# Optimization experiments

Measured on AMD Instinct MI355X. Metric: run time of the kernel, lower is better.

Reference implementation:

```python
import jax, jax.numpy as jnp
import numpy as np

B, L, D_MODEL = 4, 4096, 128
D_INNER, D_STATE, DT_RANK, D_CONV = 256, 16, 8, 4
EPS = 1e-5


def setup_inputs() -> dict:
    key = jax.random.key(0)
    ks = jax.random.split(key, 10)
    s = lambda *sh: 0.02
    inp = {
        'x': jax.random.normal(ks[0], (B, L, D_MODEL), jnp.float32),
        'norm_w': jnp.ones((D_MODEL,), jnp.float32),
        # Linear weights stored as (in, out) so y = x @ W
        'in_proj_w': jax.random.normal(ks[1], (D_MODEL, 2 * D_INNER), jnp.float32) * 0.02,
        'conv_w': jax.random.normal(ks[2], (D_INNER, D_CONV), jnp.float32) * 0.2,
        'conv_b': jnp.zeros((D_INNER,), jnp.float32),
        'x_proj_w': jax.random.normal(ks[3], (D_INNER, DT_RANK + 2 * D_STATE), jnp.float32) * 0.02,
        'dt_proj_w': jax.random.normal(ks[4], (DT_RANK, D_INNER), jnp.float32) * 0.1,
        'dt_proj_b': jnp.zeros((D_INNER,), jnp.float32),
        'A_log': jnp.log(jnp.tile(jnp.arange(1, D_STATE + 1, dtype=jnp.float32)[None, :], (D_INNER, 1))),
        'D': jnp.ones((D_INNER,), jnp.float32),
        'out_proj_w': jax.random.normal(ks[5], (D_INNER, D_MODEL), jnp.float32) * 0.02,
    }
    return inp


def _mamba_block(x, norm_w, in_proj_w, conv_w, conv_b, x_proj_w,
                 dt_proj_w, dt_proj_b, A_log, D, out_proj_w):
    b, l, d = x.shape
    # RMSNorm
    h = x * jax.lax.rsqrt(jnp.mean(x * x, axis=-1, keepdims=True) + EPS) * norm_w
    # in_proj -> split into x path and residual gate
    xr = h @ in_proj_w                      # (b, l, 2*d_inner)
    xi, res = jnp.split(xr, 2, axis=-1)
    # depthwise causal conv1d over time
    xc = jnp.transpose(xi, (0, 2, 1))       # (b, d_inner, l)
    kernel = conv_w[:, None, :]             # (d_inner, 1, d_conv)
    xc = jax.lax.conv_general_dilated(
        xc, kernel, window_strides=(1,), padding=[(D_CONV - 1, 0)],
        feature_group_count=D_INNER,
        dimension_numbers=('NCH', 'OIH', 'NCH')) + conv_b[None, :, None]
    xc = jnp.transpose(xc, (0, 2, 1))       # (b, l, d_inner)
    xc = jax.nn.silu(xc)
    # SSM parameterization
    A = -jnp.exp(A_log.astype(jnp.float32))           # (d_inner, n)
    x_dbl = xc @ x_proj_w                              # (b, l, dt_rank + 2n)
    delta = x_dbl[..., :DT_RANK]
    Bmat = x_dbl[..., DT_RANK:DT_RANK + D_STATE]       # (b, l, n)
    Cmat = x_dbl[..., DT_RANK + D_STATE:]              # (b, l, n)
    delta = jax.nn.softplus(delta @ dt_proj_w + dt_proj_b)  # (b, l, d_inner)
    # discretize
    deltaA = jnp.exp(jnp.einsum('bld,dn->bldn', delta, A))  # (b, l, d_inner, n)
    deltaB_u = delta[..., None] * Bmat[:, :, None, :] * xc[..., None]
    # selective scan over time (lax.scan replaces the Python loop)
    def step(s, inputs):
        dA_t, dBu_t, C_t = inputs
        s = dA_t * s + dBu_t                     # (b, d_inner, n)
        y_t = jnp.einsum('bdn,bn->bd', s, C_t)   # (b, d_inner)
        return s, y_t
    s0 = jnp.zeros((b, D_INNER, D_STATE), xc.dtype)
    scan_in = (jnp.transpose(deltaA, (1, 0, 2, 3)),
               jnp.transpose(deltaB_u, (1, 0, 2, 3)),
               jnp.transpose(Cmat, (1, 0, 2)))
    _, ys = jax.lax.scan(step, s0, scan_in)      # (l, b, d_inner)
    y = jnp.transpose(ys, (1, 0, 2)) + xc * D    # (b, l, d_inner)
    y = y * jax.nn.silu(res)
    return y @ out_proj_w + x                    # residual add


def reference(x, norm_w, in_proj_w, conv_w, conv_b, x_proj_w,
              dt_proj_w, dt_proj_b, A_log, D, out_proj_w):
    return _mamba_block(x, norm_w, in_proj_w, conv_w, conv_b, x_proj_w,
                        dt_proj_w, dt_proj_b, A_log, D, out_proj_w)
```

## Files before the change

kernel.cpp:

```cpp
#include <hip/hip_runtime.h>
#include <math.h>

#define B_    4
#define L_    4096
#define DM    128
#define DI    256
#define DS    16
#define DTR   8
#define XPN   (DTR + 2*DS)
#define NB    (DI + 2*DS)
#define M_    (B_*L_)
#define CHUNK 32
#define NC    (L_/CHUNK)
#define LOG2E 1.4426950408889634f
#define PREP_N (512*128 + NB*DI + DM*DI)

typedef __attribute__((ext_vector_type(8))) short bf16x8;
typedef __attribute__((ext_vector_type(4))) float f32x4;
typedef unsigned short ushort_t;

__device__ __forceinline__ ushort_t f2bf(float f) {
  unsigned int u = __float_as_uint(f);
  u += 0x7FFFu + ((u >> 16) & 1u);
  return (ushort_t)(u >> 16);
}
__device__ __forceinline__ float bf2f(ushort_t u) {
  return __uint_as_float(((unsigned int)u) << 16);
}

__global__ __launch_bounds__(256) void prep_rms_kernel(const float* __restrict__ x,
                                                       const float* __restrict__ nw,
                                                       const float* __restrict__ inW,
                                                       const float* __restrict__ Wx,
                                                       const float* __restrict__ Wdt,
                                                       const float* __restrict__ outw,
                                                       ushort_t* __restrict__ xbf,
                                                       ushort_t* __restrict__ inWt,
                                                       ushort_t* __restrict__ WbigT,
                                                       ushort_t* __restrict__ outWt) {
  if (blockIdx.x < M_ / 4) {
    int row  = blockIdx.x * 4 + (threadIdx.x >> 6);
    int lane = threadIdx.x & 63;
    const float* xp = x + (size_t)row * DM;
    float v0 = xp[lane], v1 = xp[lane + 64];
    float s = v0 * v0 + v1 * v1;
    #pragma unroll
    for (int off = 32; off > 0; off >>= 1) s += __shfl_xor(s, off);
    float r = rsqrtf(s / DM + 1e-5f);
    ushort_t* op = xbf + (size_t)row * DM;
    op[lane]      = f2bf(v0 * r * nw[lane]);
    op[lane + 64] = f2bf(v1 * r * nw[lane + 64]);
    return;
  }
  int g = (blockIdx.x - M_ / 4) * 256 + threadIdx.x;
  if (g < 512 * 128) {
    int n = g >> 7, k = g & 127;
    inWt[g] = f2bf(inW[k * 512 + n]);
  } else if (g < 512 * 128 + NB * DI) {
    int q = g - 512 * 128;
    int c = q >> 8, k = q & 255;
    float v;
    if (c < DI) {
      v = 0.f;
      #pragma unroll
      for (int j = 0; j < DTR; ++j) v = fmaf(Wx[k * XPN + j], Wdt[j * DI + c], v);
    } else {
      v = Wx[k * XPN + DTR + (c - DI)];
    }
    WbigT[q] = f2bf(v);
  } else if (g < PREP_N) {
    int q = g - (512 * 128 + NB * DI);
    int n = q >> 8, k = q & 255;
    outWt[q] = f2bf(outw[k * DM + n]);
  }
}

__global__ __launch_bounds__(256) void g1_conv_kernel(const ushort_t* __restrict__ A,
                                                      const ushort_t* __restrict__ Wt,
                                                      const float* __restrict__ cw,
                                                      const float* __restrict__ cb,
                                                      ushort_t* __restrict__ xcbf,
                                                      ushort_t* __restrict__ resbf) {
  constexpr int BM = 128, BN = 64, BK = 64, KK = 128, NT = BN / 16;
  __shared__ __align__(16) char smem_raw[35648];
  ushort_t (*Asm)[145][8] = (ushort_t (*)[145][8])smem_raw;
  ushort_t (*Bsm)[65][8]  = (ushort_t (*)[65][8])(smem_raw + 18560);
  float* T = (float*)smem_raw;
  const int tid  = threadIdx.x;
  const int wave = tid >> 6, lane = tid & 63;
  const int quad = lane >> 4, l16 = lane & 15;
  const int row0 = blockIdx.x * BM;
  const int by   = blockIdx.y;
  const int col0 = by * BN;
  const bool zpad = (row0 & (L_ - 1)) == 0;
  f32x4 acc[2][NT], acc2[NT];
  #pragma unroll
  for (int mt = 0; mt < 2; ++mt)
    #pragma unroll
    for (int nt = 0; nt < NT; ++nt) acc[mt][nt] = (f32x4){0.f, 0.f, 0.f, 0.f};
  #pragma unroll
  for (int nt = 0; nt < NT; ++nt) acc2[nt] = (f32x4){0.f, 0.f, 0.f, 0.f};

  for (int k0 = 0; k0 < KK; k0 += BK) {
    #pragma unroll
    for (int i = 0; i < 5; ++i) {
      int q = tid + i * 256;
      if (i < 4 || tid < 128) {
        int m = q >> 3, kb = q & 7;
        bf16x8 v = {0, 0, 0, 0, 0, 0, 0, 0};
        if (!(zpad && m < 16))
          v = *(const bf16x8*)(A + (size_t)(row0 - 16 + m) * KK + k0 + kb * 8);
        *(bf16x8*)(&Asm[kb][m][0]) = v;
      }
    }
    #pragma unroll
    for (int i = 0; i < 2; ++i) {
      int q = tid + i * 256;
      int n = q >> 3, kb = q & 7;
      *(bf16x8*)(&Bsm[kb][n][0]) =
          *(const bf16x8*)(Wt + (size_t)(col0 + n) * KK + k0 + kb * 8);
    }
    __syncthreads();
    #pragma unroll
    for (int ks = 0; ks < 2; ++ks) {
      bf16x8 af[2], bfr[NT];
      #pragma unroll
      for (int mt = 0; mt < 2; ++mt)
        af[mt] = *(const bf16x8*)(&Asm[ks * 4 + quad][16 + wave * 32 + mt * 16 + l16][0]);
      #pragma unroll
      for (int nt = 0; nt < NT; ++nt)
        bfr[nt] = *(const bf16x8*)(&Bsm[ks * 4 + quad][nt * 16 + l16][0]);
      #pragma unroll
      for (int mt = 0; mt < 2; ++mt)
        #pragma unroll
        for (int nt = 0; nt < NT; ++nt)
          acc[mt][nt] = __builtin_amdgcn_mfma_f32_16x16x32_bf16(af[mt], bfr[nt],
                                                                acc[mt][nt], 0, 0, 0);
      if (by < 4 && wave == 0) {
        bf16x8 ab = *(const bf16x8*)(&Asm[ks * 4 + quad][l16][0]);
        #pragma unroll
        for (int nt = 0; nt < NT; ++nt)
          acc2[nt] = __builtin_amdgcn_mfma_f32_16x16x32_bf16(ab, bfr[nt],
                                                             acc2[nt], 0, 0, 0);
      }
    }
    __syncthreads();
  }

  if (by < 4) {
    #pragma unroll
    for (int mt = 0; mt < 2; ++mt)
      #pragma unroll
      for (int nt = 0; nt < NT; ++nt)
        #pragma unroll
        for (int r = 0; r < 4; ++r)
          T[(3 + wave * 32 + mt * 16 + quad * 4 + r) * 68 + nt * 16 + l16] =
              acc[mt][nt][r];
    if (wave == 0 && quad == 3) {
      #pragma unroll
      for (int nt = 0; nt < NT; ++nt)
        #pragma unroll
        for (int r = 1; r < 4; ++r)
          T[(r - 1) * 68 + nt * 16 + l16] = acc2[nt][r];
    }
    __syncthreads();
    const int c   = tid & 63;
    const int R0  = (tid >> 6) * 32;
    const int dch = col0 + c;
    float4 w4   = *(const float4*)(cw + dch * 4);
    float bias  = cb[dch];
    float t0 = T[(R0 + 0) * 68 + c];
    float t1 = T[(R0 + 1) * 68 + c];
    float t2 = T[(R0 + 2) * 68 + c];
    for (int rr = 0; rr < 32; ++rr) {
      float t3 = T[(R0 + rr + 3) * 68 + c];
      float s = fmaf(w4.x, t0, fmaf(w4.y, t1, fmaf(w4.z, t2, fmaf(w4.w, t3, bias))));
      float v = s / (1.f + __expf(-s));
      xcbf[(size_t)(row0 + R0 + rr) * DI + dch] = f2bf(v);
      t0 = t1; t1 = t2; t2 = t3;
    }
  } else {
    const int cr = col0 - 256;
    #pragma unroll
    for (int mt = 0; mt < 2; ++mt)
      #pragma unroll
      for (int nt = 0; nt < NT; ++nt) {
        int col   = cr + nt * 16 + l16;
        int rbase = row0 + wave * 32 + mt * 16 + quad * 4;
        #pragma unroll
        for (int r = 0; r < 4; ++r)
          resbf[(size_t)(rbase + r) * DI + col] = f2bf(acc[mt][nt][r]);
      }
  }
}

__global__ __launch_bounds__(512, 4) void scanA_kernel(
    const ushort_t* __restrict__ xcbf, const ushort_t* __restrict__ WbigT,
    const float* __restrict__ bdt, const float* __restrict__ Alog,
    ushort_t* __restrict__ deltab, ushort_t* __restrict__ Bmb,
    ushort_t* __restrict__ Cmb, float2* __restrict__ PS) {
  __shared__ __align__(16) ushort_t Asm[32][33][8];
  __shared__ float T[32][257];
  __shared__ float Bs[32][17], Cs[32][17];
  const int tid  = threadIdx.x;
  const int wave = tid >> 6, lane = tid & 63;
  const int quad = lane >> 4, l16 = lane & 15;
  const int b = blockIdx.x >> 7, c = blockIdx.x & (NC - 1);
  const size_t rowbase = (size_t)b * L_ + (size_t)c * CHUNK;
  const int d  = (wave << 5) | (lane & 31);
  const int nh = lane >> 5;
  const int n0 = nh * 8;

  {
    int m = tid & 31, kb = tid >> 5;
    *(bf16x8*)(&Asm[kb][m][0]) =
        *(const bf16x8*)(xcbf + (rowbase + m) * DI + kb * 8);
    *(bf16x8*)(&Asm[kb + 16][m][0]) =
        *(const bf16x8*)(xcbf + (rowbase + m) * DI + (kb + 16) * 8);
  }
  __syncthreads();

  for (int tp = wave; tp < 36; tp += 8) {
    int mt = tp / 18, nt = tp % 18;
    f32x4 acc = {0.f, 0.f, 0.f, 0.f};
    #pragma unroll
    for (int ks = 0; ks < 8; ++ks) {
      bf16x8 af = *(const bf16x8*)(&Asm[ks * 4 + quad][mt * 16 + l16][0]);
      bf16x8 bf = *(const bf16x8*)(WbigT + (size_t)(nt * 16 + l16) * DI + ks * 32 + quad * 8);
      acc = __builtin_amdgcn_mfma_f32_16x16x32_bf16(af, bf, acc, 0, 0, 0);
    }
    int row = mt * 16 + quad * 4;
    if (nt < 16) {
      int col = nt * 16 + l16;
      float bb = bdt[col];
      #pragma unroll
      for (int r = 0; r < 4; ++r) {
        float v = acc[r] + bb;
        T[row + r][col] = (v > 20.f) ? v : log1pf(__expf(v));
      }
    } else if (nt == 16) {
      #pragma unroll
      for (int r = 0; r < 4; ++r) Bs[row + r][l16] = acc[r];
    } else {
      #pragma unroll
      for (int r = 0; r < 4; ++r) Cs[row + r][l16] = acc[r];
    }
  }
  __syncthreads();

  #pragma unroll
  for (int i = 0; i < 8; ++i) {
    int idx2 = tid + i * 512;
    int row = idx2 >> 7, cp = idx2 & 127;
    unsigned int pk = (unsigned int)f2bf(T[row][2 * cp]) |
                      ((unsigned int)f2bf(T[row][2 * cp + 1]) << 16);
    *(unsigned int*)(deltab + (rowbase + row) * DI + 2 * cp) = pk;
  }
  {
    int row = tid >> 4, n = tid & 15;
    Bmb[rowbase * DS + tid] = f2bf(Bs[row][n]);
    Cmb[rowbase * DS + tid] = f2bf(Cs[row][n]);
  }

  float c0 = -__expf(Alog[d * DS]) * LOG2E;
  float aln[8];
  #pragma unroll
  for (int j = 0; j < 8; ++j) aln[j] = -__expf(Alog[d * DS + n0 + j]) * LOG2E;
  bool geom = true;
  #pragma unroll
  for (int j = 0; j < 8; ++j)
    geom = geom && (fabsf(aln[j] - (n0 + j + 1) * c0) <= 1e-3f * fabsf(aln[j]));

  float P[8], S[8];
  #pragma unroll
  for (int j = 0; j < 8; ++j) { P[j] = 1.f; S[j] = 0.f; }
  for (int t = 0; t < CHUNK; ++t) {
    float dl = T[t][d];
    float xv = bf2f(Asm[d >> 3][t][d & 7]);
    float du = dl * xv;
    if (geom) {
      float e1 = exp2f(dl * c0);
      float a;
      if (nh) { float e2 = e1 * e1, e4 = e2 * e2; a = e4 * e4 * e1; }
      else a = e1;
      #pragma unroll
      for (int j = 0; j < 8; ++j) {
        P[j] *= a;
        S[j] = fmaf(a, S[j], du * Bs[t][n0 + j]);
        a *= e1;
      }
    } else {
      #pragma unroll
      for (int j = 0; j < 8; ++j) {
        float a = exp2f(dl * aln[j]);
        P[j] *= a;
        S[j] = fmaf(a, S[j], du * Bs[t][n0 + j]);
      }
    }
  }
  size_t ob = ((size_t)(b * NC + c) << 12) + ((nh * 256 + d) << 3);
  float4* p4 = (float4*)(PS + ob);
  p4[0] = make_float4(P[0], S[0], P[1], S[1]);
  p4[1] = make_float4(P[2], S[2], P[3], S[3]);
  p4[2] = make_float4(P[4], S[4], P[5], S[5]);
  p4[3] = make_float4(P[6], S[6], P[7], S[7]);
}

__global__ __launch_bounds__(64) void scanB_kernel(const float2* __restrict__ PS,
                                                   float* __restrict__ sinit) {
  int g  = blockIdx.x * 64 + threadIdx.x;
  int b  = g >> 12;
  int dn = g & 4095;
  float s = 0.f;
  #pragma unroll 8
  for (int c = 0; c < NC; ++c) {
    size_t idx = ((size_t)(b * NC + c) << 12) + dn;
    sinit[idx] = s;
    float2 v = PS[idx];
    s = fmaf(v.x, s, v.y);
  }
}

__global__ __launch_bounds__(512, 4) void scanC_kernel(
    const ushort_t* __restrict__ deltab, const ushort_t* __restrict__ xcbf,
    const ushort_t* __restrict__ Bmb, const ushort_t* __restrict__ Cmb,
    const float* __restrict__ Alog, const float* __restrict__ Dp,
    const ushort_t* __restrict__ resbf, const float* __restrict__ sinit,
    const ushort_t* __restrict__ outWt, const float* __restrict__ x,
    float* __restrict__ out) {
  __shared__ float Bs[32][17], Cs[32][17];
  __shared__ __align__(16) ushort_t y2s[32][264];
  const int tid  = threadIdx.x;
  const int wave = tid >> 6, lane = tid & 63;
  const int quad = lane >> 4, l16 = lane & 15;
  const int b = blockIdx.x >> 7, c = blockIdx.x & (NC - 1);
  const size_t rowbase = (size_t)b * L_ + (size_t)c * CHUNK;
  const int d  = (wave << 5) | (lane & 31);
  const int nh = lane >> 5;
  const int n0 = nh * 8;
  {
    int row = tid >> 4, n = tid & 15;
    Bs[row][n] = bf2f(Bmb[rowbase * DS + tid]);
    Cs[row][n] = bf2f(Cmb[rowbase * DS + tid]);
  }
  float c0 = -__expf(Alog[d * DS]) * LOG2E;
  float aln[8];
  #pragma unroll
  for (int j = 0; j < 8; ++j) aln[j] = -__expf(Alog[d * DS + n0 + j]) * LOG2E;
  bool geom = true;
  #pragma unroll
  for (int j = 0; j < 8; ++j)
    geom = geom && (fabsf(aln[j] - (n0 + j + 1) * c0) <= 1e-3f * fabsf(aln[j]));
  const float Dd = Dp[d];
  float S[8];
  {
    size_t ib = ((size_t)(b * NC + c) << 12) + ((nh * 256 + d) << 3);
    float4 v0 = *(const float4*)(sinit + ib);
    float4 v1 = *(const float4*)(sinit + ib + 4);
    S[0] = v0.x; S[1] = v0.y; S[2] = v0.z; S[3] = v0.w;
    S[4] = v1.x; S[5] = v1.y; S[6] = v1.z; S[7] = v1.w;
  }
  __syncthreads();
  for (int t = 0; t < CHUNK; ++t) {
    float dl = bf2f(deltab[(rowbase + t) * DI + d]);
    float xv = bf2f(xcbf[(rowbase + t) * DI + d]);
    float du = dl * xv;
    float y = 0.f;
    if (geom) {
      float e1 = exp2f(dl * c0);
      float a;
      if (nh) { float e2 = e1 * e1, e4 = e2 * e2; a = e4 * e4 * e1; }
      else a = e1;
      #pragma unroll
      for (int j = 0; j < 8; ++j) {
        S[j] = fmaf(a, S[j], du * Bs[t][n0 + j]);
        y = fmaf(S[j], Cs[t][n0 + j], y);
        a *= e1;
      }
    } else {
      #pragma unroll
      for (int j = 0; j < 8; ++j) {
        float a = exp2f(dl * aln[j]);
        S[j] = fmaf(a, S[j], du * Bs[t][n0 + j]);
        y = fmaf(S[j], Cs[t][n0 + j], y);
      }
    }
    float yo = __shfl_xor(y, 32);
    if (nh == 0) {
      float rv = bf2f(resbf[(rowbase + t) * DI + d]);
      float yt = y + yo + xv * Dd;
      float sil = rv / (1.f + __expf(-rv));
      y2s[t][d] = f2bf(yt * sil);
    }
  }
  __syncthreads();
  #pragma unroll
  for (int mt = 0; mt < 2; ++mt) {
    f32x4 acc = {0.f, 0.f, 0.f, 0.f};
    #pragma unroll
    for (int ks = 0; ks < 8; ++ks) {
      bf16x8 af = *(const bf16x8*)(&y2s[mt * 16 + l16][ks * 32 + quad * 8]);
      bf16x8 bf = *(const bf16x8*)(outWt + (size_t)(wave * 16 + l16) * DI + ks * 32 + quad * 8);
      acc = __builtin_amdgcn_mfma_f32_16x16x32_bf16(af, bf, acc, 0, 0, 0);
    }
    int col = wave * 16 + l16;
    size_t rb = rowbase + mt * 16 + quad * 4;
    #pragma unroll
    for (int r = 0; r < 4; ++r)
      out[(rb + r) * DM + col] = acc[r] + x[(rb + r) * DM + col];
  }
}

extern "C" void kernel_launch(void* const* d_in, const int* in_sizes, int n_in,
                              void* d_out, int out_size, void* d_ws, size_t ws_size,
                              hipStream_t stream) {
  const float* x      = (const float*)d_in[0];
  const float* norm_w = (const float*)d_in[1];
  const float* inW    = (const float*)d_in[2];
  const float* convw  = (const float*)d_in[3];
  const float* convb  = (const float*)d_in[4];
  const float* xprojw = (const float*)d_in[5];
  const float* dtw    = (const float*)d_in[6];
  const float* dtb    = (const float*)d_in[7];
  const float* alog   = (const float*)d_in[8];
  const float* Dp     = (const float*)d_in[9];
  const float* outw   = (const float*)d_in[10];
  float* out = (float*)d_out;

  const size_t CS = (size_t)B_ * NC * DI * DS;
  float2* PS    = (float2*)d_ws;
  float* sinit  = (float*)(PS + CS);
  ushort_t* bfbase = (ushort_t*)(sinit + CS);
  ushort_t* xbf    = bfbase;
  ushort_t* xcbf   = xbf + (size_t)M_ * DM;
  ushort_t* resbf  = xcbf + (size_t)M_ * DI;
  ushort_t* deltab = resbf + (size_t)M_ * DI;
  ushort_t* Bmb    = deltab + (size_t)M_ * DI;
  ushort_t* Cmb    = Bmb + (size_t)M_ * DS;
  ushort_t* inWt   = Cmb + (size_t)M_ * DS;
  ushort_t* WbigT  = inWt + 512 * 128;
  ushort_t* outWt  = WbigT + NB * DI;

  prep_rms_kernel<<<M_ / 4 + (PREP_N + 255) / 256, 256, 0, stream>>>(
      x, norm_w, inW, xprojw, dtw, outw, xbf, inWt, WbigT, outWt);
  g1_conv_kernel<<<dim3(M_ / 128, 8), 256, 0, stream>>>(
      xbf, inWt, convw, convb, xcbf, resbf);
  scanA_kernel<<<B_ * NC, 512, 0, stream>>>(
      xcbf, WbigT, dtb, alog, deltab, Bmb, Cmb, PS);
  scanB_kernel<<<(B_ * DI * DS) / 64, 64, 0, stream>>>(PS, sinit);
  scanC_kernel<<<B_ * NC, 512, 0, stream>>>(
      deltab, xcbf, Bmb, Cmb, alog, Dp, resbf, sinit, outWt, x, out);
}
```

Measured before the change: 169.4 us.

## Fuse RMSNorm into in_proj GEMM and pack scan chunk summaries as bf16

RMSNorm moves out of the prep kernel and into the in_proj/conv GEMM. Each block now reads fp32 x directly, computes per-row scales, and writes normalized bf16 rows into shared memory across the full K=128, which removes the intermediate xbf buffer round trip. The cost is that each block redoes the norm for its rows and halo, 8 column blocks per row tile, and needs more LDS. The per-chunk (P,S) summaries passed from scanA to scanB are also packed into bf16 pairs to halve that traffic, which adds precision loss to the carried state, and the scanB unroll rises from 8 to 16.

```diff
diff --git a/kernel.cpp b/kernel.cpp
--- a/kernel.cpp
+++ b/kernel.cpp
@@ -13,11 +13,12 @@
 #define CHUNK 32
 #define NC    (L_/CHUNK)
 #define LOG2E 1.4426950408889634f
-#define PREP_N (512*128 + NB*DI + DM*DI)
+#define PREPW_N (512*128 + NB*DI + DM*DI)
 
 typedef __attribute__((ext_vector_type(8))) short bf16x8;
 typedef __attribute__((ext_vector_type(4))) float f32x4;
 typedef unsigned short ushort_t;
+typedef unsigned int uint_t;
 
 __device__ __forceinline__ ushort_t f2bf(float f) {
   unsigned int u = __float_as_uint(f);
@@ -27,32 +28,18 @@
 __device__ __forceinline__ float bf2f(ushort_t u) {
   return __uint_as_float(((unsigned int)u) << 16);
 }
-
-__global__ __launch_bounds__(256) void prep_rms_kernel(const float* __restrict__ x,
-                                                       const float* __restrict__ nw,
-                                                       const float* __restrict__ inW,
-                                                       const float* __restrict__ Wx,
-                                                       const float* __restrict__ Wdt,
-                                                       const float* __restrict__ outw,
-                                                       ushort_t* __restrict__ xbf,
-                                                       ushort_t* __restrict__ inWt,
-                                                       ushort_t* __restrict__ WbigT,
-                                                       ushort_t* __restrict__ outWt) {
-  if (blockIdx.x < M_ / 4) {
-    int row  = blockIdx.x * 4 + (threadIdx.x >> 6);
-    int lane = threadIdx.x & 63;
-    const float* xp = x + (size_t)row * DM;
-    float v0 = xp[lane], v1 = xp[lane + 64];
-    float s = v0 * v0 + v1 * v1;
-    #pragma unroll
-    for (int off = 32; off > 0; off >>= 1) s += __shfl_xor(s, off);
-    float r = rsqrtf(s / DM + 1e-5f);
-    ushort_t* op = xbf + (size_t)row * DM;
-    op[lane]      = f2bf(v0 * r * nw[lane]);
-    op[lane + 64] = f2bf(v1 * r * nw[lane + 64]);
-    return;
-  }
-  int g = (blockIdx.x - M_ / 4) * 256 + threadIdx.x;
+__device__ __forceinline__ uint_t pack2(float p, float s) {
+  return (uint_t)f2bf(p) | ((uint_t)f2bf(s) << 16);
+}
+
+__global__ __launch_bounds__(256) void prep_w_kernel(const float* __restrict__ inW,
+                                                     const float* __restrict__ Wx,
+                                                     const float* __restrict__ Wdt,
+                                                     const float* __restrict__ outw,
+                                                     ushort_t* __restrict__ inWt,
+                                                     ushort_t* __restrict__ WbigT,
+                                                     ushort_t* __restrict__ outWt) {
+  int g = blockIdx.x * 256 + threadIdx.x;
   if (g < 512 * 128) {
     int n = g >> 7, k = g & 127;
     inWt[g] = f2bf(inW[k * 512 + n]);
@@ -68,31 +55,68 @@
       v = Wx[k * XPN + DTR + (c - DI)];
     }
     WbigT[q] = f2bf(v);
-  } else if (g < PREP_N) {
+  } else if (g < PREPW_N) {
     int q = g - (512 * 128 + NB * DI);
     int n = q >> 8, k = q & 255;
     outWt[q] = f2bf(outw[k * DM + n]);
   }
 }
 
-__global__ __launch_bounds__(256) void g1_conv_kernel(const ushort_t* __restrict__ A,
+__global__ __launch_bounds__(256) void g1_conv_kernel(const float* __restrict__ x,
+                                                      const float* __restrict__ nw,
                                                       const ushort_t* __restrict__ Wt,
                                                       const float* __restrict__ cw,
                                                       const float* __restrict__ cb,
                                                       ushort_t* __restrict__ xcbf,
                                                       ushort_t* __restrict__ resbf) {
-  constexpr int BM = 128, BN = 64, BK = 64, KK = 128, NT = BN / 16;
-  __shared__ __align__(16) char smem_raw[35648];
+  constexpr int NT = 4;
+  __shared__ __align__(16) char smem_raw[46528];
   ushort_t (*Asm)[145][8] = (ushort_t (*)[145][8])smem_raw;
-  ushort_t (*Bsm)[65][8]  = (ushort_t (*)[65][8])(smem_raw + 18560);
-  float* T = (float*)smem_raw;
+  ushort_t (*Bsm)[65][8]  = (ushort_t (*)[65][8])(smem_raw + 37120);
+  float* scl = (float*)(smem_raw + 45440);
+  float* nwS = (float*)(smem_raw + 46016);
+  float* T   = (float*)smem_raw;
   const int tid  = threadIdx.x;
   const int wave = tid >> 6, lane = tid & 63;
   const int quad = lane >> 4, l16 = lane & 15;
-  const int row0 = blockIdx.x * BM;
+  const int row0 = blockIdx.x * 128;
   const int by   = blockIdx.y;
-  const int col0 = by * BN;
+  const int col0 = by * 64;
   const bool zpad = (row0 & (L_ - 1)) == 0;
+
+  if (tid < 32) ((float4*)nwS)[tid] = ((const float4*)nw)[tid];
+  for (int i = 0; i < 18; ++i) {
+    int p = wave * 18 + i;
+    int m = 2 * p + (lane >> 5);
+    float4 v = make_float4(0.f, 0.f, 0.f, 0.f);
+    if (!(zpad && m < 16))
+      v = *(const float4*)(x + (size_t)(row0 - 16 + m) * DM + (lane & 31) * 4);
+    float s = v.x * v.x + v.y * v.y + v.z * v.z + v.w * v.w;
+    #pragma unroll
+    for (int off = 16; off > 0; off >>= 1) s += __shfl_xor(s, off);
+    if ((lane & 31) == 0) scl[m] = rsqrtf(s / DM + 1e-5f);
+  }
+  __syncthreads();
+
+  #pragma unroll
+  for (int i = 0; i < 9; ++i) {
+    int q = tid + i * 256;
+    int m = q >> 4, kb = q & 15;
+    bf16x8 v8 = {0, 0, 0, 0, 0, 0, 0, 0};
+    if (!(zpad && m < 16)) {
+      const float* xp = x + (size_t)(row0 - 16 + m) * DM + kb * 8;
+      float4 a = ((const float4*)xp)[0], b = ((const float4*)xp)[1];
+      float sc = scl[m];
+      float4 n0 = *(const float4*)(nwS + kb * 8);
+      float4 n1 = *(const float4*)(nwS + kb * 8 + 4);
+      v8[0] = (short)f2bf(a.x * sc * n0.x); v8[1] = (short)f2bf(a.y * sc * n0.y);
+      v8[2] = (short)f2bf(a.z * sc * n0.z); v8[3] = (short)f2bf(a.w * sc * n0.w);
+      v8[4] = (short)f2bf(b.x * sc * n1.x); v8[5] = (short)f2bf(b.y * sc * n1.y);
+      v8[6] = (short)f2bf(b.z * sc * n1.z); v8[7] = (short)f2bf(b.w * sc * n1.w);
+    }
+    *(bf16x8*)(&Asm[kb][m][0]) = v8;
+  }
+
   f32x4 acc[2][NT], acc2[NT];
   #pragma unroll
   for (int mt = 0; mt < 2; ++mt)
@@ -101,32 +125,23 @@
   #pragma unroll
   for (int nt = 0; nt < NT; ++nt) acc2[nt] = (f32x4){0.f, 0.f, 0.f, 0.f};
 
-  for (int k0 = 0; k0 < KK; k0 += BK) {
-    #pragma unroll
-    for (int i = 0; i < 5; ++i) {
-      int q = tid + i * 256;
-      if (i < 4 || tid < 128) {
-        int m = q >> 3, kb = q & 7;
-        bf16x8 v = {0, 0, 0, 0, 0, 0, 0, 0};
-        if (!(zpad && m < 16))
-          v = *(const bf16x8*)(A + (size_t)(row0 - 16 + m) * KK + k0 + kb * 8);
-        *(bf16x8*)(&Asm[kb][m][0]) = v;
-      }
-    }
+  #pragma unroll
+  for (int k0i = 0; k0i < 2; ++k0i) {
     #pragma unroll
     for (int i = 0; i < 2; ++i) {
       int q = tid + i * 256;
       int n = q >> 3, kb = q & 7;
       *(bf16x8*)(&Bsm[kb][n][0]) =
-          *(const bf16x8*)(Wt + (size_t)(col0 + n) * KK + k0 + kb * 8);
+          *(const bf16x8*)(Wt + (size_t)(col0 + n) * DM + k0i * 64 + kb * 8);
     }
     __syncthreads();
     #pragma unroll
     for (int ks = 0; ks < 2; ++ks) {
+      int kbg = k0i * 8 + ks * 4 + quad;
       bf16x8 af[2], bfr[NT];
       #pragma unroll
       for (int mt = 0; mt < 2; ++mt)
-        af[mt] = *(const bf16x8*)(&Asm[ks * 4 + quad][16 + wave * 32 + mt * 16 + l16][0]);
+        af[mt] = *(const bf16x8*)(&Asm[kbg][16 + wave * 32 + mt * 16 + l16][0]);
       #pragma unroll
       for (int nt = 0; nt < NT; ++nt)
         bfr[nt] = *(const bf16x8*)(&Bsm[ks * 4 + quad][nt * 16 + l16][0]);
@@ -137,7 +152,7 @@
           acc[mt][nt] = __builtin_amdgcn_mfma_f32_16x16x32_bf16(af[mt], bfr[nt],
                                                                 acc[mt][nt], 0, 0, 0);
       if (by < 4 && wave == 0) {
-        bf16x8 ab = *(const bf16x8*)(&Asm[ks * 4 + quad][l16][0]);
+        bf16x8 ab = *(const bf16x8*)(&Asm[kbg][l16][0]);
         #pragma unroll
         for (int nt = 0; nt < NT; ++nt)
           acc2[nt] = __builtin_amdgcn_mfma_f32_16x16x32_bf16(ab, bfr[nt],
@@ -198,7 +213,7 @@
     const ushort_t* __restrict__ xcbf, const ushort_t* __restrict__ WbigT,
     const float* __restrict__ bdt, const float* __restrict__ Alog,
     ushort_t* __restrict__ deltab, ushort_t* __restrict__ Bmb,
-    ushort_t* __restrict__ Cmb, float2* __restrict__ PS) {
+    ushort_t* __restrict__ Cmb, uint_t* __restrict__ PS) {
   __shared__ __align__(16) ushort_t Asm[32][33][8];
   __shared__ float T[32][257];
   __shared__ float Bs[32][17], Cs[32][17];
@@ -299,25 +314,27 @@
     }
   }
   size_t ob = ((size_t)(b * NC + c) << 12) + ((nh * 256 + d) << 3);
-  float4* p4 = (float4*)(PS + ob);
-  p4[0] = make_float4(P[0], S[0], P[1], S[1]);
-  p4[1] = make_float4(P[2], S[2], P[3], S[3]);
-  p4[2] = make_float4(P[4], S[4], P[5], S[5]);
-  p4[3] = make_float4(P[6], S[6], P[7], S[7]);
-}
-
-__global__ __launch_bounds__(64) void scanB_kernel(const float2* __restrict__ PS,
+  uint4 w0, w1;
+  w0.x = pack2(P[0], S[0]); w0.y = pack2(P[1], S[1]);
+  w0.z = pack2(P[2], S[2]); w0.w = pack2(P[3], S[3]);
+  w1.x = pack2(P[4], S[4]); w1.y = pack2(P[5], S[5]);
+  w1.z = pack2(P[6], S[6]); w1.w = pack2(P[7], S[7]);
+  *(uint4*)(PS + ob)     = w0;
+  *(uint4*)(PS + ob + 4) = w1;
+}
+
+__global__ __launch_bounds__(64) void scanB_kernel(const uint_t* __restrict__ PS,
                                                    float* __restrict__ sinit) {
   int g  = blockIdx.x * 64 + threadIdx.x;
   int b  = g >> 12;
   int dn = g & 4095;
   float s = 0.f;
-  #pragma unroll 8
+  #pragma unroll 16
   for (int c = 0; c < NC; ++c) {
     size_t idx = ((size_t)(b * NC + c) << 12) + dn;
     sinit[idx] = s;
-    float2 v = PS[idx];
-    s = fmaf(v.x, s, v.y);
+    uint_t v = PS[idx];
+    s = fmaf(bf2f((ushort_t)(v & 0xffffu)), s, bf2f((ushort_t)(v >> 16)));
   }
 }
 
@@ -428,11 +445,10 @@
   float* out = (float*)d_out;
 
   const size_t CS = (size_t)B_ * NC * DI * DS;
-  float2* PS    = (float2*)d_ws;
+  uint_t* PS    = (uint_t*)d_ws;
   float* sinit  = (float*)(PS + CS);
   ushort_t* bfbase = (ushort_t*)(sinit + CS);
-  ushort_t* xbf    = bfbase;
-  ushort_t* xcbf   = xbf + (size_t)M_ * DM;
+  ushort_t* xcbf   = bfbase;
   ushort_t* resbf  = xcbf + (size_t)M_ * DI;
   ushort_t* deltab = resbf + (size_t)M_ * DI;
   ushort_t* Bmb    = deltab + (size_t)M_ * DI;
@@ -441,10 +457,10 @@
   ushort_t* WbigT  = inWt + 512 * 128;
   ushort_t* outWt  = WbigT + NB * DI;
 
-  prep_rms_kernel<<<M_ / 4 + (PREP_N + 255) / 256, 256, 0, stream>>>(
-      x, norm_w, inW, xprojw, dtw, outw, xbf, inWt, WbigT, outWt);
+  prep_w_kernel<<<(PREPW_N + 255) / 256, 256, 0, stream>>>(
+      inW, xprojw, dtw, outw, inWt, WbigT, outWt);
   g1_conv_kernel<<<dim3(M_ / 128, 8), 256, 0, stream>>>(
-      xbf, inWt, convw, convb, xcbf, resbf);
+      x, norm_w, inWt, convw, convb, xcbf, resbf);
   scanA_kernel<<<B_ * NC, 512, 0, stream>>>(
       xcbf, WbigT, dtb, alog, deltab, Bmb, Cmb, PS);
   scanB_kernel<<<(B_ * DI * DS) / 64, 64, 0, stream>>>(PS, sinit);
```

Measured after the change: 180.6 us. 6.6% more time.
